# Performance work log

Hardware: AMD Instinct MI355X
Metric: run time of the kernel (lower is better)

The kernel has to match this reference:

```python
import jax, jax.numpy as jnp
import numpy as np

T = 3072          # packed tokens (B==1 varlen)
DIM = 1024        # model_dim
H = 8             # num_heads
D = 128           # head_dim
GATE_IN = 16      # gate projections read first 16 channels of x
ATTN_SCALE = 0.1  # Yarn attn_scale
BM = 1408         # sliding-window size (block_size * ws)


def _rms_norm(x, eps=1e-6):
    return x * jax.lax.rsqrt(jnp.mean(x * x, axis=-1, keepdims=True) + eps)


def _rotary(x, cos, sin):
    # x: [B,T,H,D]; cos/sin: [T,D//2]
    c = cos[None, :x.shape[1], None, :]
    s = sin[None, :x.shape[1], None, :]
    x1, x2 = jnp.split(x, 2, axis=-1)
    return jnp.concatenate([x1 * c + x2 * s, -x1 * s + x2 * c], axis=-1)


def setup_inputs() -> dict:
    key = jax.random.key(0)
    ks = jax.random.split(key, 6)
    x = jax.random.normal(ks[0], (1, T, DIM), dtype=jnp.float32)
    qkvo_w = 0.02 * jax.random.normal(ks[1], (4 * DIM, DIM), dtype=jnp.float32)
    sa_lambdas = jnp.ones((2,), dtype=jnp.float32)
    ve = 0.5 * jax.random.normal(ks[2], (T, DIM), dtype=jnp.float32)
    attn_gate_w = 0.1 * jax.random.normal(ks[3], (H, GATE_IN), dtype=jnp.float32)
    ve_gate_w = 0.1 * jax.random.normal(ks[4], (H, GATE_IN), dtype=jnp.float32)
    # Yarn rotary tables: half the freq channels are zero (NoPE half)
    angular_freq = (1.0 / 1024.0) ** jnp.linspace(0, 1, D // 4, dtype=jnp.float32)
    angular_freq = jnp.concatenate([angular_freq, jnp.zeros(D // 4, dtype=jnp.float32)])
    theta = jnp.arange(T, dtype=jnp.float32)[:, None] * angular_freq[None, :]
    cos, sin = jnp.cos(theta), jnp.sin(theta)
    # two packed sequences of length T//2 (cu_seqlens = [0, T//2, T])
    seg_ids = jnp.concatenate([jnp.zeros(T // 2, jnp.int32), jnp.ones(T // 2, jnp.int32)])
    return {"x": x, "qkvo_w": qkvo_w, "sa_lambdas": sa_lambdas, "ve": ve,
            "attn_gate_w": attn_gate_w, "ve_gate_w": ve_gate_w,
            "cos": cos, "sin": sin, "seg_ids": seg_ids, "bm_size": BM}


def reference(x, qkvo_w, sa_lambdas, ve, attn_gate_w, ve_gate_w, cos, sin, seg_ids, bm_size):
    B, Tt, dim = x.shape
    nh = attn_gate_w.shape[0]
    hd = dim // nh
    # fused qkv projection with learned lambda scaling
    qkv = x @ (sa_lambdas[0] * qkvo_w[:3 * dim]).T              # [B,T,3*dim]
    qkv = qkv.reshape(B, Tt, 3 * nh, hd)
    q, k, v = jnp.split(qkv, 3, axis=2)                          # each [B,T,H,D]
    q, k = _rms_norm(q), _rms_norm(k)
    q, k = _rotary(q, cos, sin), _rotary(k, cos, sin)
    # key_offset: channels [D/4:D/2] and [3D/4:D] take previous token's keys
    k_prev = jnp.concatenate([k[:, :1], k[:, :-1]], axis=1)
    k = jnp.concatenate([k[..., :hd // 4], k_prev[..., hd // 4:hd // 2],
                         k[..., hd // 2:3 * hd // 4], k_prev[..., 3 * hd // 4:]], axis=-1)
    # value-embedding gate: 2*sigmoid(x[:,:,:16] @ W^T)
    ve_gate = 2.0 * jax.nn.sigmoid(x[..., :ve_gate_w.shape[-1]] @ ve_gate_w.T)  # [B,T,H]
    v = v + ve_gate[..., None] * ve.reshape(B, Tt, nh, hd)
    # windowed causal varlen attention (dense reference for flash_attn_varlen)
    scores = jnp.einsum('bthd,bshd->bhts', q, k) * ATTN_SCALE
    t_idx = jnp.arange(Tt)
    mask = ((t_idx[None, :] <= t_idx[:, None])
            & (t_idx[None, :] >= t_idx[:, None] - bm_size)
            & (seg_ids[None, :] == seg_ids[:, None]))
    scores = jnp.where(mask[None, None], scores, -jnp.inf)
    p = jax.nn.softmax(scores, axis=-1)
    y = jnp.einsum('bhts,bshd->bthd', p, v)
    # attention output gate
    gate = jax.nn.sigmoid(x[..., :attn_gate_w.shape[-1]] @ attn_gate_w.T)      # [B,T,H]
    y = y * gate[..., None]
    y = y.reshape(B, Tt, dim)
    return y @ (sa_lambdas[1] * qkvo_w[3 * dim:]).T
```

## Files before the change

kernel.cpp:

```cpp
#include <hip/hip_runtime.h>
#include <hip/hip_bf16.h>
#include <stdint.h>

#define TSEQ 3072
#define DIMM 1024
#define NH   8
#define HD   128
#define QBLK 32

typedef float f32x4 __attribute__((ext_vector_type(4)));
typedef short s16x8 __attribute__((ext_vector_type(8)));
typedef unsigned short u16;

static __device__ __forceinline__ u16 f2b(float f) {
  union { float f; unsigned u; } a; a.f = f;
  unsigned r = a.u + 0x7FFFu + ((a.u >> 16) & 1u);
  return (u16)(r >> 16);
}
static __device__ __forceinline__ void gload_lds16(const void* g, void* l) {
  __builtin_amdgcn_global_load_lds(
      (const __attribute__((address_space(1))) unsigned int*)(unsigned long long)g,
      (__attribute__((address_space(3))) unsigned int*)(unsigned long long)l,
      16, 0, 0);
}
static __device__ __forceinline__ void bar() {
  asm volatile("" ::: "memory");
  __builtin_amdgcn_s_barrier();
  asm volatile("" ::: "memory");
}
#define SWAIT(n) asm volatile("s_waitcnt vmcnt(" #n ")" ::: "memory")

__global__ __launch_bounds__(256) void k_convert(
    const float* __restrict__ x, const float* __restrict__ w,
    const float* __restrict__ lam,
    u16* __restrict__ xb, u16* __restrict__ wb)
{
  const int NX = TSEQ * DIMM;
  const int NW = 4 * DIMM * DIMM;
  const float l0 = lam[0], l1 = lam[1];
  const int n4 = (NX + NW) >> 2;
  for (int j = blockIdx.x * 256 + threadIdx.x; j < n4; j += gridDim.x * 256) {
    const int e = j << 2;
    float4 v; u16* dst; float s;
    if (e < NX) { v = *(const float4*)(x + e); dst = xb + e; s = 1.f; }
    else {
      const int we = e - NX;
      v = *(const float4*)(w + we);
      dst = wb + we;
      s = (we < 3 * DIMM * DIMM) ? l0 : l1;
    }
    dst[0] = f2b(v.x * s); dst[1] = f2b(v.y * s);
    dst[2] = f2b(v.z * s); dst[3] = f2b(v.w * s);
  }
}

__global__ __launch_bounds__(256) void k_gemm_nt(
    const u16* __restrict__ A, const u16* __restrict__ B,
    float* __restrict__ C, int M, int N, int K)
{
  __shared__ u16 As[128 * 64];
  __shared__ u16 Bs[128 * 64];
  const int tid = threadIdx.x;
  const int lane = tid & 63, wv = tid >> 6;
  const int m0 = blockIdx.y * 128, n0 = blockIdx.x * 128;
  const int wm = (wv >> 1) * 64, wn = (wv & 1) * 64;
  const int c0 = lane & 15, r0 = (lane >> 4) * 4, koff = (lane >> 4) * 8;

  f32x4 acc[4][4];
  #pragma unroll
  for (int i = 0; i < 4; i++)
    #pragma unroll
    for (int j = 0; j < 4; j++) acc[i][j] = (f32x4){0.f, 0.f, 0.f, 0.f};

  const int srow = tid >> 3;
  const int scol = (tid & 7) * 8;
  const size_t a_base = (size_t)(m0 + srow) * K + scol;
  const size_t b_base = (size_t)(n0 + srow) * K + scol;

  for (int kt = 0; kt < K; kt += 64) {
    __syncthreads();
    #pragma unroll
    for (int i = 0; i < 4; i++) {
      gload_lds16(A + a_base + (size_t)(i * 32) * K + kt, (char*)As + i * 4096 + tid * 16);
      gload_lds16(B + b_base + (size_t)(i * 32) * K + kt, (char*)Bs + i * 4096 + tid * 16);
    }
    __syncthreads();
    #pragma unroll
    for (int kk = 0; kk < 2; kk++) {
      s16x8 af[4], bf[4];
      #pragma unroll
      for (int i = 0; i < 4; i++) {
        af[i] = *(const s16x8*)&As[(wm + i * 16 + c0) * 64 + kk * 32 + koff];
        bf[i] = *(const s16x8*)&Bs[(wn + i * 16 + c0) * 64 + kk * 32 + koff];
      }
      #pragma unroll
      for (int i = 0; i < 4; i++)
        #pragma unroll
        for (int j = 0; j < 4; j++)
          acc[i][j] = __builtin_amdgcn_mfma_f32_16x16x32_bf16(af[i], bf[j], acc[i][j], 0, 0, 0);
    }
  }
  #pragma unroll
  for (int i = 0; i < 4; i++)
    #pragma unroll
    for (int j = 0; j < 4; j++) {
      float* cp = C + (size_t)(m0 + wm + i * 16 + r0) * N + n0 + wn + j * 16 + c0;
      #pragma unroll
      for (int r = 0; r < 4; r++) cp[(size_t)r * N] = acc[i][j][r];
    }
}

__global__ __launch_bounds__(256) void k_prep(
    const float* __restrict__ qkv, const float* __restrict__ x,
    const float* __restrict__ ve, const float* __restrict__ cosb,
    const float* __restrict__ sinb, const float* __restrict__ gwa,
    const float* __restrict__ gwv,
    u16* __restrict__ Qg, u16* __restrict__ Kg, u16* __restrict__ Vtmp,
    float* __restrict__ gateA)
{
  const int gid = blockIdx.x * 4 + (threadIdx.x >> 6);
  const int lane = threadIdx.x & 63;
  const int h = gid / TSEQ;
  const int t = gid - h * TSEQ;
  const int tp = (t == 0) ? 0 : t - 1;

  const float* qrow = qkv + (size_t)t * (3 * DIMM) + h * HD;
  const float* krow = qrow + DIMM;
  const float* vrow = qrow + 2 * DIMM;
  const float* prow = qkv + (size_t)tp * (3 * DIMM) + DIMM + h * HD;

  float q1 = qrow[lane], q2 = qrow[lane + 64];
  float k1 = krow[lane], k2 = krow[lane + 64];
  float p1 = prow[lane], p2 = prow[lane + 64];

  float sq = q1 * q1 + q2 * q2, sk = k1 * k1 + k2 * k2, sp = p1 * p1 + p2 * p2;
  #pragma unroll
  for (int m = 1; m < 64; m <<= 1) {
    sq += __shfl_xor(sq, m, 64);
    sk += __shfl_xor(sk, m, 64);
    sp += __shfl_xor(sp, m, 64);
  }
  const float rq = rsqrtf(sq * (1.f / 128.f) + 1e-6f);
  const float rk = rsqrtf(sk * (1.f / 128.f) + 1e-6f);
  const float rp = rsqrtf(sp * (1.f / 128.f) + 1e-6f);
  q1 *= rq; q2 *= rq; k1 *= rk; k2 *= rk; p1 *= rp; p2 *= rp;

  const float c  = cosb[t * 64 + lane],  s  = sinb[t * 64 + lane];
  const float cp = cosb[tp * 64 + lane], spv = sinb[tp * 64 + lane];
  const float qo1 =  q1 * c + q2 * s,   qo2 = -q1 * s + q2 * c;
  const float ko1 =  k1 * c + k2 * s,   ko2 = -k1 * s + k2 * c;
  const float po1 =  p1 * cp + p2 * spv, po2 = -p1 * spv + p2 * cp;
  const float m1 = (lane < 32) ? ko1 : po1;
  const float m2 = (lane < 32) ? ko2 : po2;

  const size_t qkbase = ((size_t)h * TSEQ + t) * HD + lane;
  Qg[qkbase] = f2b(qo1); Qg[qkbase + 64] = f2b(qo2);
  Kg[qkbase] = f2b(m1);  Kg[qkbase + 64] = f2b(m2);

  float dv = 0.f, da = 0.f;
  #pragma unroll
  for (int g = 0; g < 16; g++) {
    const float xv = x[(size_t)t * DIMM + g];
    dv += xv * gwv[h * 16 + g];
    da += xv * gwa[h * 16 + g];
  }
  const float vg = 2.f / (1.f + __expf(-dv));
  const float v1 = vrow[lane]      + vg * ve[(size_t)t * DIMM + h * HD + lane];
  const float v2 = vrow[lane + 64] + vg * ve[(size_t)t * DIMM + h * HD + lane + 64];
  u16* vt = Vtmp + ((size_t)h * TSEQ + t) * HD;
  vt[lane] = f2b(v1); vt[lane + 64] = f2b(v2);
  if (lane == 0) gateA[h * TSEQ + t] = 1.f / (1.f + __expf(-da));
}

__global__ __launch_bounds__(256) void k_vtrans(
    const u16* __restrict__ Vtmp, u16* __restrict__ VT)
{
  __shared__ u16 tile[64][68];
  const int h  = blockIdx.z;
  const int d0 = blockIdx.y * 64;
  const int t0 = blockIdx.x * 64;
  const int tid = threadIdx.x;
  const int rr = tid >> 3, cc = (tid & 7) * 8;
  #pragma unroll
  for (int p = 0; p < 2; p++) {
    const int r = rr + p * 32;
    const s16x8 v = *(const s16x8*)(Vtmp + ((size_t)h * TSEQ + t0 + r) * HD + d0 + cc);
    #pragma unroll
    for (int j = 0; j < 8; j++) tile[r][cc + j] = ((const u16*)&v)[j];
  }
  __syncthreads();
  #pragma unroll
  for (int p = 0; p < 2; p++) {
    const int r = rr + p * 32;
    s16x8 v;
    #pragma unroll
    for (int j = 0; j < 8; j++) ((u16*)&v)[j] = tile[cc + j][r];
    *(s16x8*)(VT + ((size_t)h * HD + d0 + r) * TSEQ + t0 + cc) = v;
  }
}

__global__ __launch_bounds__(128) void k_attn(
    const u16* __restrict__ Qg, const u16* __restrict__ Kg,
    const u16* __restrict__ VTg, const float* __restrict__ gateA,
    const int* __restrict__ seg, const int* __restrict__ bmp,
    u16* __restrict__ Y)
{
  __shared__ u16 Ks[2][64 * HD];
  __shared__ u16 Vs[HD * 64];
  __shared__ u16 Ps[2][16 * 64];

  const int tid = threadIdx.x, lane = tid & 63, wv = tid >> 6;
  const int h = blockIdx.y;
  const int q0 = blockIdx.x * QBLK;
  const int qw = q0 + wv * 16;
  const int bm = bmp[0];
  const int r0 = (lane >> 4) * 4, c0 = lane & 15;
  const int koff = (lane >> 4) * 8;

  s16x8 qf[4];
  {
    const u16* qp = Qg + ((size_t)h * TSEQ + qw + c0) * HD + koff;
    #pragma unroll
    for (int kk = 0; kk < 4; kk++) qf[kk] = *(const s16x8*)(qp + kk * 32);
  }

  int qt[4]; int qseg[4]; float qgate[4];
  #pragma unroll
  for (int r = 0; r < 4; r++) {
    qt[r] = qw + r0 + r;
    qseg[r] = seg[qt[r]];
    qgate[r] = gateA[h * TSEQ + qt[r]];
  }
  const int segw_lo = seg[qw], segw_hi = seg[qw + 15];

  const int seg_q = seg[q0];
  int lo = 0, hi = q0;
  while (lo < hi) { const int mid = (lo + hi) >> 1; if (seg[mid] < seg_q) lo = mid + 1; else hi = mid; }
  int s_begin = q0 - bm; if (s_begin < lo) s_begin = lo; if (s_begin < 0) s_begin = 0;
  s_begin &= ~63;
  const int s_end = q0 + QBLK;

  f32x4 o[8];
  #pragma unroll
  for (int i = 0; i < 8; i++) o[i] = (f32x4){0.f, 0.f, 0.f, 0.f};
  float mrow[4] = {-1e30f, -1e30f, -1e30f, -1e30f};
  float lrow[4] = {0.f, 0.f, 0.f, 0.f};

  auto stageK = [&](int buf, int s0k) {
    #pragma unroll
    for (int i = 0; i < 8; i++) {
      const int L = tid * 16 + i * 2048;
      const int kr = L >> 8;
      const int kc = (L & 255) ^ ((kr & 7) << 4);
      gload_lds16(Kg + ((size_t)h * TSEQ + s0k + kr) * HD + (kc >> 1), (char*)Ks[buf] + L);
    }
  };
  auto stageV = [&](int s0v) {
    #pragma unroll
    for (int i = 0; i < 8; i++) {
      const int L = tid * 16 + i * 2048;
      const int vr = L >> 7;
      const int vc = (L & 127) ^ ((vr & 7) << 4);
      gload_lds16(VTg + ((size_t)h * HD + vr) * TSEQ + s0v + (vc >> 1), (char*)Vs + L);
    }
  };

  stageK(0, s_begin);
  int cur = 0;

  for (int s0 = s_begin; s0 < s_end; s0 += 64) {
    bar();
    stageV(s0);
    int sn = s0 + 64; if (sn >= s_end) sn = s0;
    stageK(cur ^ 1, sn);
    SWAIT(16);
    bar();

    const char* kbase = (const char*)Ks[cur];
    f32x4 sv[4];
    #pragma unroll
    for (int n = 0; n < 4; n++) {
      sv[n] = (f32x4){0.f, 0.f, 0.f, 0.f};
      const int krow = n * 16 + c0;
      #pragma unroll
      for (int kk = 0; kk < 4; kk++) {
        const int kbyte = (krow << 8) + ((((kk * 32 + koff) << 1)) ^ ((krow & 7) << 4));
        const s16x8 kf = *(const s16x8*)(kbase + kbyte);
        sv[n] = __builtin_amdgcn_mfma_f32_16x16x32_bf16(qf[kk], kf, sv[n], 0, 0, 0);
      }
    }

    const bool interior = (s0 + 64 <= qw) && (s0 >= qw + 15 - bm) &&
                          (seg[s0] == seg[s0 + 63]) && (seg[s0] == segw_lo) &&
                          (segw_lo == segw_hi);
    if (interior) {
      #pragma unroll
      for (int n = 0; n < 4; n++)
        #pragma unroll
        for (int r = 0; r < 4; r++) sv[n][r] *= 0.1f;
    } else {
      #pragma unroll
      for (int n = 0; n < 4; n++) {
        const int key = s0 + n * 16 + c0;
        const int ks = seg[key];
        #pragma unroll
        for (int r = 0; r < 4; r++) {
          const bool ok = (key <= qt[r]) && (key >= qt[r] - bm) && (ks == qseg[r]);
          sv[n][r] = ok ? sv[n][r] * 0.1f : -1e30f;
        }
      }
    }

    float pm[4];
    #pragma unroll
    for (int r = 0; r < 4; r++)
      pm[r] = fmaxf(fmaxf(sv[0][r], sv[1][r]), fmaxf(sv[2][r], sv[3][r]));
    #pragma unroll
    for (int m = 1; m < 16; m <<= 1)
      #pragma unroll
      for (int r = 0; r < 4; r++) pm[r] = fmaxf(pm[r], __shfl_xor(pm[r], m, 64));

    float scl[4], rs[4];
    #pragma unroll
    for (int r = 0; r < 4; r++) {
      const float mn = fmaxf(mrow[r], pm[r]);
      scl[r] = __expf(mrow[r] - mn);
      mrow[r] = mn;
      rs[r] = 0.f;
    }
    u16 pb[4][4];
    #pragma unroll
    for (int n = 0; n < 4; n++)
      #pragma unroll
      for (int r = 0; r < 4; r++) {
        const float p = (sv[n][r] < -0.5e30f) ? 0.f : __expf(sv[n][r] - mrow[r]);
        rs[r] += p;
        pb[n][r] = f2b(p);
      }
    #pragma unroll
    for (int m = 1; m < 16; m <<= 1)
      #pragma unroll
      for (int r = 0; r < 4; r++) rs[r] += __shfl_xor(rs[r], m, 64);
    #pragma unroll
    for (int r = 0; r < 4; r++) lrow[r] = lrow[r] * scl[r] + rs[r];
    #pragma unroll
    for (int i = 0; i < 8; i++)
      #pragma unroll
      for (int r = 0; r < 4; r++) o[i][r] *= scl[r];

    char* pbase = (char*)Ps[wv];
    #pragma unroll
    for (int n = 0; n < 4; n++)
      #pragma unroll
      for (int r = 0; r < 4; r++) {
        const int row = r0 + r;
        const int byt = (row << 7) + ((((n * 16 + c0) << 1)) ^ ((row & 7) << 4));
        *(u16*)(pbase + byt) = pb[n][r];
      }

    SWAIT(8);
    bar();

    #pragma unroll
    for (int kc = 0; kc < 2; kc++) {
      const int pbyte = (c0 << 7) + ((((kc * 32 + koff) << 1)) ^ ((c0 & 7) << 4));
      const s16x8 pf = *(const s16x8*)(pbase + pbyte);
      #pragma unroll
      for (int nf = 0; nf < 8; nf++) {
        const int vrow = nf * 16 + c0;
        const int vbyte = (vrow << 7) + ((((kc * 32 + koff) << 1)) ^ ((vrow & 7) << 4));
        const s16x8 vf = *(const s16x8*)((const char*)Vs + vbyte);
        o[nf] = __builtin_amdgcn_mfma_f32_16x16x32_bf16(pf, vf, o[nf], 0, 0, 0);
      }
    }
    cur ^= 1;
  }

  SWAIT(0);

  #pragma unroll
  for (int r = 0; r < 4; r++) {
    const float inv = (lrow[r] > 0.f) ? (qgate[r] / lrow[r]) : 0.f;
    #pragma unroll
    for (int nf = 0; nf < 8; nf++)
      Y[(size_t)qt[r] * DIMM + h * HD + nf * 16 + c0] = f2b(o[nf][r] * inv);
  }
}

extern "C" void kernel_launch(void* const* d_in, const int* in_sizes, int n_in,
                              void* d_out, int out_size, void* d_ws, size_t ws_size,
                              hipStream_t stream) {
  const float* x    = (const float*)d_in[0];
  const float* qkvo = (const float*)d_in[1];
  const float* lam  = (const float*)d_in[2];
  const float* ve   = (const float*)d_in[3];
  const float* gwa  = (const float*)d_in[4];
  const float* gwv  = (const float*)d_in[5];
  const float* cosb = (const float*)d_in[6];
  const float* sinb = (const float*)d_in[7];
  const int*   seg  = (const int*)d_in[8];
  const int*   bm   = (const int*)d_in[9];
  float* out = (float*)d_out;

  char* ws = (char*)d_ws;
  size_t off = 0;
  auto alloc = [&](size_t bytes) -> void* {
    void* p = ws + off;
    off += (bytes + 255) & ~(size_t)255;
    return p;
  };
  u16*   xb    = (u16*)alloc((size_t)TSEQ * DIMM * 2);
  u16*   wb    = (u16*)alloc((size_t)4 * DIMM * DIMM * 2);
  float* qkv   = (float*)alloc((size_t)TSEQ * 3 * DIMM * 4);
  u16*   Qg    = (u16*)alloc((size_t)NH * TSEQ * HD * 2);
  u16*   Kg    = (u16*)alloc((size_t)NH * TSEQ * HD * 2);
  u16*   Vtmp  = (u16*)alloc((size_t)NH * TSEQ * HD * 2);
  u16*   VTg   = (u16*)alloc((size_t)NH * HD * TSEQ * 2);
  float* gateA = (float*)alloc((size_t)NH * TSEQ * 4);
  u16*   Yg    = (u16*)alloc((size_t)TSEQ * DIMM * 2);

  k_convert<<<2048, 256, 0, stream>>>(x, qkvo, lam, xb, wb);
  k_gemm_nt<<<dim3(24, 24), 256, 0, stream>>>(xb, wb, qkv, TSEQ, 3 * DIMM, DIMM);
  k_prep<<<NH * TSEQ / 4, 256, 0, stream>>>(qkv, x, ve, cosb, sinb, gwa, gwv, Qg, Kg, Vtmp, gateA);
  k_vtrans<<<dim3(TSEQ / 64, HD / 64, NH), 256, 0, stream>>>(Vtmp, VTg);
  k_attn<<<dim3(TSEQ / QBLK, NH), 128, 0, stream>>>(Qg, Kg, VTg, gateA, seg, bm, Yg);
  k_gemm_nt<<<dim3(DIMM / 128, 24), 256, 0, stream>>>(Yg, wb + (size_t)3 * DIMM * DIMM, out, TSEQ, DIMM, DIMM);
}
```

Baseline: 245.8 us.

## Fuse V transpose into prep kernel, fold attn scale into Q, reverse attention block order

The prep kernel now handles 64 tokens per block for one head and stages V in shared memory, then writes it out transposed. This removes the separate transpose kernel and the Vtmp round trip through global memory. The 0.1 attention scale is folded into Q before the bf16 cast, which drops a multiply per score in the attention loop but changes rounding slightly. Attention blocks are launched on a 1D grid, heaviest query blocks first with heads interleaved, to improve load balance across the causal work.

Result: no change. 245.8 us (-0.0%).

```diff
diff --git a/kernel.cpp b/kernel.cpp
--- a/kernel.cpp
+++ b/kernel.cpp
@@ -115,87 +115,75 @@
     const float* __restrict__ ve, const float* __restrict__ cosb,
     const float* __restrict__ sinb, const float* __restrict__ gwa,
     const float* __restrict__ gwv,
-    u16* __restrict__ Qg, u16* __restrict__ Kg, u16* __restrict__ Vtmp,
+    u16* __restrict__ Qg, u16* __restrict__ Kg, u16* __restrict__ VTg,
     float* __restrict__ gateA)
 {
-  const int gid = blockIdx.x * 4 + (threadIdx.x >> 6);
-  const int lane = threadIdx.x & 63;
-  const int h = gid / TSEQ;
-  const int t = gid - h * TSEQ;
-  const int tp = (t == 0) ? 0 : t - 1;
-
-  const float* qrow = qkv + (size_t)t * (3 * DIMM) + h * HD;
-  const float* krow = qrow + DIMM;
-  const float* vrow = qrow + 2 * DIMM;
-  const float* prow = qkv + (size_t)tp * (3 * DIMM) + DIMM + h * HD;
-
-  float q1 = qrow[lane], q2 = qrow[lane + 64];
-  float k1 = krow[lane], k2 = krow[lane + 64];
-  float p1 = prow[lane], p2 = prow[lane + 64];
-
-  float sq = q1 * q1 + q2 * q2, sk = k1 * k1 + k2 * k2, sp = p1 * p1 + p2 * p2;
-  #pragma unroll
-  for (int m = 1; m < 64; m <<= 1) {
-    sq += __shfl_xor(sq, m, 64);
-    sk += __shfl_xor(sk, m, 64);
-    sp += __shfl_xor(sp, m, 64);
-  }
-  const float rq = rsqrtf(sq * (1.f / 128.f) + 1e-6f);
-  const float rk = rsqrtf(sk * (1.f / 128.f) + 1e-6f);
-  const float rp = rsqrtf(sp * (1.f / 128.f) + 1e-6f);
-  q1 *= rq; q2 *= rq; k1 *= rk; k2 *= rk; p1 *= rp; p2 *= rp;
-
-  const float c  = cosb[t * 64 + lane],  s  = sinb[t * 64 + lane];
-  const float cp = cosb[tp * 64 + lane], spv = sinb[tp * 64 + lane];
-  const float qo1 =  q1 * c + q2 * s,   qo2 = -q1 * s + q2 * c;
-  const float ko1 =  k1 * c + k2 * s,   ko2 = -k1 * s + k2 * c;
-  const float po1 =  p1 * cp + p2 * spv, po2 = -p1 * spv + p2 * cp;
-  const float m1 = (lane < 32) ? ko1 : po1;
-  const float m2 = (lane < 32) ? ko2 : po2;
-
-  const size_t qkbase = ((size_t)h * TSEQ + t) * HD + lane;
-  Qg[qkbase] = f2b(qo1); Qg[qkbase + 64] = f2b(qo2);
-  Kg[qkbase] = f2b(m1);  Kg[qkbase + 64] = f2b(m2);
-
-  float dv = 0.f, da = 0.f;
-  #pragma unroll
-  for (int g = 0; g < 16; g++) {
-    const float xv = x[(size_t)t * DIMM + g];
-    dv += xv * gwv[h * 16 + g];
-    da += xv * gwa[h * 16 + g];
-  }
-  const float vg = 2.f / (1.f + __expf(-dv));
-  const float v1 = vrow[lane]      + vg * ve[(size_t)t * DIMM + h * HD + lane];
-  const float v2 = vrow[lane + 64] + vg * ve[(size_t)t * DIMM + h * HD + lane + 64];
-  u16* vt = Vtmp + ((size_t)h * TSEQ + t) * HD;
-  vt[lane] = f2b(v1); vt[lane + 64] = f2b(v2);
-  if (lane == 0) gateA[h * TSEQ + t] = 1.f / (1.f + __expf(-da));
-}
-
-__global__ __launch_bounds__(256) void k_vtrans(
-    const u16* __restrict__ Vtmp, u16* __restrict__ VT)
-{
-  __shared__ u16 tile[64][68];
-  const int h  = blockIdx.z;
-  const int d0 = blockIdx.y * 64;
+  __shared__ u16 vtile[64][130];
+  const int tid = threadIdx.x;
+  const int lane = tid & 63, w = tid >> 6;
+  const int h = blockIdx.y;
   const int t0 = blockIdx.x * 64;
-  const int tid = threadIdx.x;
-  const int rr = tid >> 3, cc = (tid & 7) * 8;
-  #pragma unroll
-  for (int p = 0; p < 2; p++) {
-    const int r = rr + p * 32;
-    const s16x8 v = *(const s16x8*)(Vtmp + ((size_t)h * TSEQ + t0 + r) * HD + d0 + cc);
-    #pragma unroll
-    for (int j = 0; j < 8; j++) tile[r][cc + j] = ((const u16*)&v)[j];
+
+  for (int it = 0; it < 16; ++it) {
+    const int tt = it * 4 + w;
+    const int t = t0 + tt;
+    const int tp = (t == 0) ? 0 : t - 1;
+
+    const float* qrow = qkv + (size_t)t * (3 * DIMM) + h * HD;
+    const float* krow = qrow + DIMM;
+    const float* vrow = qrow + 2 * DIMM;
+    const float* prow = qkv + (size_t)tp * (3 * DIMM) + DIMM + h * HD;
+
+    float q1 = qrow[lane], q2 = qrow[lane + 64];
+    float k1 = krow[lane], k2 = krow[lane + 64];
+    float p1 = prow[lane], p2 = prow[lane + 64];
+
+    float sq = q1 * q1 + q2 * q2, sk = k1 * k1 + k2 * k2, sp = p1 * p1 + p2 * p2;
+    #pragma unroll
+    for (int m = 1; m < 64; m <<= 1) {
+      sq += __shfl_xor(sq, m, 64);
+      sk += __shfl_xor(sk, m, 64);
+      sp += __shfl_xor(sp, m, 64);
+    }
+    const float rq = rsqrtf(sq * (1.f / 128.f) + 1e-6f);
+    const float rk = rsqrtf(sk * (1.f / 128.f) + 1e-6f);
+    const float rp = rsqrtf(sp * (1.f / 128.f) + 1e-6f);
+    q1 *= rq; q2 *= rq; k1 *= rk; k2 *= rk; p1 *= rp; p2 *= rp;
+
+    const float c  = cosb[t * 64 + lane],  s  = sinb[t * 64 + lane];
+    const float cp = cosb[tp * 64 + lane], spv = sinb[tp * 64 + lane];
+    const float qo1 =  q1 * c + q2 * s,   qo2 = -q1 * s + q2 * c;
+    const float ko1 =  k1 * c + k2 * s,   ko2 = -k1 * s + k2 * c;
+    const float po1 =  p1 * cp + p2 * spv, po2 = -p1 * spv + p2 * cp;
+    const float m1 = (lane < 32) ? ko1 : po1;
+    const float m2 = (lane < 32) ? ko2 : po2;
+
+    const size_t qkbase = ((size_t)h * TSEQ + t) * HD + lane;
+    Qg[qkbase] = f2b(qo1 * 0.1f); Qg[qkbase + 64] = f2b(qo2 * 0.1f);
+    Kg[qkbase] = f2b(m1);  Kg[qkbase + 64] = f2b(m2);
+
+    float dv = 0.f, da = 0.f;
+    #pragma unroll
+    for (int g = 0; g < 16; g++) {
+      const float xv = x[(size_t)t * DIMM + g];
+      dv += xv * gwv[h * 16 + g];
+      da += xv * gwa[h * 16 + g];
+    }
+    const float vg = 2.f / (1.f + __expf(-dv));
+    const float v1 = vrow[lane]      + vg * ve[(size_t)t * DIMM + h * HD + lane];
+    const float v2 = vrow[lane + 64] + vg * ve[(size_t)t * DIMM + h * HD + lane + 64];
+    vtile[tt][lane] = f2b(v1); vtile[tt][lane + 64] = f2b(v2);
+    if (lane == 0) gateA[h * TSEQ + t] = 1.f / (1.f + __expf(-da));
   }
   __syncthreads();
   #pragma unroll
-  for (int p = 0; p < 2; p++) {
-    const int r = rr + p * 32;
+  for (int rep = 0; rep < 4; ++rep) {
+    const int d = rep * 32 + (tid >> 3);
+    const int cc = (tid & 7) * 8;
     s16x8 v;
     #pragma unroll
-    for (int j = 0; j < 8; j++) ((u16*)&v)[j] = tile[cc + j][r];
-    *(s16x8*)(VT + ((size_t)h * HD + d0 + r) * TSEQ + t0 + cc) = v;
+    for (int j = 0; j < 8; j++) ((u16*)&v)[j] = vtile[cc + j][d];
+    *(s16x8*)(VTg + ((size_t)h * HD + d) * TSEQ + t0 + cc) = v;
   }
 }
 
@@ -210,8 +198,10 @@
   __shared__ u16 Ps[2][16 * 64];
 
   const int tid = threadIdx.x, lane = tid & 63, wv = tid >> 6;
-  const int h = blockIdx.y;
-  const int q0 = blockIdx.x * QBLK;
+  const int bid = blockIdx.x;
+  const int h = bid & 7;
+  const int qidx = (TSEQ / QBLK - 1) - (bid >> 3);
+  const int q0 = qidx * QBLK;
   const int qw = q0 + wv * 16;
   const int bm = bmp[0];
   const int r0 = (lane >> 4) * 4, c0 = lane & 15;
@@ -293,12 +283,7 @@
     const bool interior = (s0 + 64 <= qw) && (s0 >= qw + 15 - bm) &&
                           (seg[s0] == seg[s0 + 63]) && (seg[s0] == segw_lo) &&
                           (segw_lo == segw_hi);
-    if (interior) {
-      #pragma unroll
-      for (int n = 0; n < 4; n++)
-        #pragma unroll
-        for (int r = 0; r < 4; r++) sv[n][r] *= 0.1f;
-    } else {
+    if (!interior) {
       #pragma unroll
       for (int n = 0; n < 4; n++) {
         const int key = s0 + n * 16 + c0;
@@ -306,7 +291,7 @@
         #pragma unroll
         for (int r = 0; r < 4; r++) {
           const bool ok = (key <= qt[r]) && (key >= qt[r] - bm) && (ks == qseg[r]);
-          sv[n][r] = ok ? sv[n][r] * 0.1f : -1e30f;
+          sv[n][r] = ok ? sv[n][r] : -1e30f;
         }
       }
     }
@@ -414,15 +399,13 @@
   float* qkv   = (float*)alloc((size_t)TSEQ * 3 * DIMM * 4);
   u16*   Qg    = (u16*)alloc((size_t)NH * TSEQ * HD * 2);
   u16*   Kg    = (u16*)alloc((size_t)NH * TSEQ * HD * 2);
-  u16*   Vtmp  = (u16*)alloc((size_t)NH * TSEQ * HD * 2);
   u16*   VTg   = (u16*)alloc((size_t)NH * HD * TSEQ * 2);
   float* gateA = (float*)alloc((size_t)NH * TSEQ * 4);
   u16*   Yg    = (u16*)alloc((size_t)TSEQ * DIMM * 2);
 
   k_convert<<<2048, 256, 0, stream>>>(x, qkvo, lam, xb, wb);
   k_gemm_nt<<<dim3(24, 24), 256, 0, stream>>>(xb, wb, qkv, TSEQ, 3 * DIMM, DIMM);
-  k_prep<<<NH * TSEQ / 4, 256, 0, stream>>>(qkv, x, ve, cosb, sinb, gwa, gwv, Qg, Kg, Vtmp, gateA);
-  k_vtrans<<<dim3(TSEQ / 64, HD / 64, NH), 256, 0, stream>>>(Vtmp, VTg);
-  k_attn<<<dim3(TSEQ / QBLK, NH), 128, 0, stream>>>(Qg, Kg, VTg, gateA, seg, bm, Yg);
+  k_prep<<<dim3(TSEQ / 64, NH), 256, 0, stream>>>(qkv, x, ve, cosb, sinb, gwa, gwv, Qg, Kg, VTg, gateA);
+  k_attn<<<dim3(NH * TSEQ / QBLK), 128, 0, stream>>>(Qg, Kg, VTg, gateA, seg, bm, Yg);
   k_gemm_nt<<<dim3(DIMM / 128, 24), 256, 0, stream>>>(Yg, wb + (size_t)3 * DIMM * DIMM, out, TSEQ, DIMM, DIMM);
 }
```
